# Kernel optimization log

Hardware: AMD Instinct MI355X
Metric: run time of the kernel (lower is better)

Reference implementation:

```python
import jax, jax.numpy as jnp
import numpy as np

E, H, L, B = 2048, 32, 1024, 4
S = E // H  # 64
DM, DD = 32, 64


def _ln(x, w, b, eps=1e-5):
    m = x.mean(-1, keepdims=True)
    v = ((x - m) ** 2).mean(-1, keepdims=True)
    return (x - m) / jnp.sqrt(v + eps) * w + b


def setup_inputs() -> dict:
    key = jax.random.key(0)
    ks = jax.random.split(key, 24)
    sc = 0.02  # weight scale for stability
    d = {
        'x': jax.random.normal(ks[0], (B, L, E), jnp.float32),
        'state': jax.random.normal(ks[1], (B, 2 + S, E), jnp.float32) * 0.1,
        'ln1_w': jnp.ones((E,), jnp.float32), 'ln1_b': jnp.zeros((E,), jnp.float32),
        'ln2_w': jnp.ones((E,), jnp.float32), 'ln2_b': jnp.zeros((E,), jnp.float32),
        'maa_x': jax.random.normal(ks[2], (E,), jnp.float32) * 0.1,
        'maa_w1': jax.random.normal(ks[3], (E, 5 * DM), jnp.float32) * sc,
        'maa_w2': jax.random.normal(ks[4], (5, DM, E), jnp.float32) * sc,
        'maa_stack': jax.random.normal(ks[5], (1, 5, E), jnp.float32) * 0.1,
        'time_decay': jax.random.normal(ks[6], (E,), jnp.float32) * 0.5,
        'td_w1': jax.random.normal(ks[7], (E, DD), jnp.float32) * sc,
        'td_w2': jax.random.normal(ks[8], (DD, E), jnp.float32) * sc,
        'u': jax.random.normal(ks[9], (H, S, 1), jnp.float32) * 0.1,
        'Wr': jax.random.normal(ks[10], (E, E), jnp.float32) * sc,
        'Wk': jax.random.normal(ks[11], (E, E), jnp.float32) * sc,
        'Wv': jax.random.normal(ks[12], (E, E), jnp.float32) * sc,
        'Wg': jax.random.normal(ks[13], (E, E), jnp.float32) * sc,
        'Wo': jax.random.normal(ks[14], (E, E), jnp.float32) * sc,
        'gn_w': jnp.ones((E,), jnp.float32), 'gn_b': jnp.zeros((E,), jnp.float32),
        'ffn_maa_k': jax.random.normal(ks[15], (E,), jnp.float32) * 0.1,
        'ffn_maa_r': jax.random.normal(ks[16], (E,), jnp.float32) * 0.1,
        'Wfk': jax.random.normal(ks[17], (E, E), jnp.float32) * sc,
        'Wfr': jax.random.normal(ks[18], (E, E), jnp.float32) * sc,
        'Wfv': jax.random.normal(ks[19], (E, E), jnp.float32) * sc,
    }
    return d


def _block(x, state, ln1_w, ln1_b, ln2_w, ln2_b, maa_x, maa_w1, maa_w2, maa_stack,
           time_decay, td_w1, td_w2, u, Wr, Wk, Wv, Wg, Wo, gn_w, gn_b,
           ffn_maa_k, ffn_maa_r, Wfk, Wfr, Wfv):
    b, l, e = x.shape
    h = u.shape[0]
    s_ = e // h
    # ---- time mixing (parallel over L, sequential WKV scan) ----
    xa = _ln(x, ln1_w, ln1_b)
    # token shift: sx[t] = x[t-1] - x[t], seeded from state row 1
    sx = jnp.concatenate([state[:, 1:2] - xa[:, :1], xa[:, :-1] - xa[:, 1:]], axis=1)
    xxx = jnp.tanh((xa + sx * maa_x) @ maa_w1).reshape(b, l, 5, DM)
    xxx = jnp.einsum('blfd,fde->blfe', xxx, maa_w2)            # [B,L,5,E]
    xm = xa[:, :, None] + sx[:, :, None] * (maa_stack + xxx)   # [B,L,5,E]
    xk, xw, xv, xr, xg = (xm[:, :, j] for j in range(5))       # stack order: k,w,v,r,g
    w = jnp.exp(-jnp.exp(time_decay + jnp.tanh(xw @ td_w1) @ td_w2)).reshape(b, l, h, s_)
    r = (xr @ Wr.T).reshape(b, l, h, s_)
    k = (xk @ Wk.T).reshape(b, l, h, s_)
    v = (xv @ Wv.T).reshape(b, l, h, s_)
    g = jax.nn.silu(xg @ Wg.T)                                 # [B,L,E]
    s0 = state[:, 2:2 + s_].reshape(b, h, s_, s_)              # per-head WKV state

    def step(s, rkvw):
        r_t, k_t, v_t, w_t = rkvw                              # each [B,H,S]
        a = k_t[..., :, None] * v_t[..., None, :]              # outer product [B,H,S,S]
        out = jnp.einsum('bhi,bhij->bhj', r_t, u * a + s)      # [B,H,S]
        s = a + w_t[..., :, None] * s
        return s, out

    rkvw = tuple(jnp.moveaxis(t, 1, 0) for t in (r, k, v, w))  # [L,B,H,S]
    _, out = jax.lax.scan(step, s0, rkvw)
    out = jnp.moveaxis(out, 0, 1).reshape(b, l, e)             # [B,L,E]
    # group norm over heads (eps=1e-5)
    og = out.reshape(b, l, h, s_)
    m = og.mean(-1, keepdims=True)
    va = ((og - m) ** 2).mean(-1, keepdims=True)
    og = ((og - m) / jnp.sqrt(va + 1e-5)).reshape(b, l, e) * gn_w + gn_b
    x1 = x + (og * g) @ Wo.T
    # ---- channel mixing ----
    xc = _ln(x1, ln2_w, ln2_b)
    sx2 = jnp.concatenate([state[:, 0:1] - xc[:, :1], xc[:, :-1] - xc[:, 1:]], axis=1)
    xk2 = xc + sx2 * ffn_maa_k
    xr2 = xc + sx2 * ffn_maa_r
    rr = jax.nn.sigmoid(xr2 @ Wfr.T)
    kk = jnp.square(jax.nn.relu(xk2 @ Wfk.T))
    return x1 + rr * (kk @ Wfv.T)


def reference(x, state, ln1_w, ln1_b, ln2_w, ln2_b, maa_x, maa_w1, maa_w2, maa_stack,
              time_decay, td_w1, td_w2, u, Wr, Wk, Wv, Wg, Wo, gn_w, gn_b,
              ffn_maa_k, ffn_maa_r, Wfk, Wfr, Wfv):
    return _block(x, state, ln1_w, ln1_b, ln2_w, ln2_b, maa_x, maa_w1, maa_w2, maa_stack,
                  time_decay, td_w1, td_w2, u, Wr, Wk, Wv, Wg, Wo, gn_w, gn_b,
                  ffn_maa_k, ffn_maa_r, Wfk, Wfr, Wfv)
```

## Files before the change

### kernel.cpp

```cpp
#include <hip/hip_runtime.h>


#define E     2048
#define LL    1024
#define HHH   32
#define SSS   64
#define NBL   4096
#define NBLE  8388608

typedef short bf16x8 __attribute__((ext_vector_type(8)));
typedef float f32x4  __attribute__((ext_vector_type(4)));
using u16 = unsigned short;

__device__ __forceinline__ u16 f2b(float f) {
    union { float f; unsigned int u; } c; c.f = f;
    unsigned int u = c.u;
    unsigned int r = (u + 0x7fffu + ((u >> 16) & 1u)) >> 16;
    return (u16)r;
}
__device__ __forceinline__ float b2f(u16 b) {
    union { unsigned int u; float f; } c; c.u = ((unsigned int)b) << 16; return c.f;
}

__device__ __forceinline__ float wave_sum(float v) {
#pragma unroll
    for (int m = 32; m >= 1; m >>= 1) v += __shfl_xor(v, m, 64);
    return v;
}

__device__ __forceinline__ void gl_lds16(const void* g, void* l) {
    __builtin_amdgcn_global_load_lds((const __attribute__((address_space(1))) unsigned int*)g,
                                     (__attribute__((address_space(3))) unsigned int*)l, 16, 0, 0);
}


__global__ __launch_bounds__(256) void k_convert(const float* __restrict__ in,
                                                 u16* __restrict__ out, int n) {
    int i = (blockIdx.x * 256 + threadIdx.x) * 4;
    if (i >= n) return;
    float4 v = *reinterpret_cast<const float4*>(in + i);
    ushort4 o = make_ushort4(f2b(v.x), f2b(v.y), f2b(v.z), f2b(v.w));
    *reinterpret_cast<ushort4*>(out + i) = o;
}

__global__ __launch_bounds__(256) void k_transpose(const float* __restrict__ in,
                                                   u16* __restrict__ out, int R, int C) {
    int i = blockIdx.x * 256 + threadIdx.x;
    if (i >= R * C) return;
    int r = i / C, c = i - r * C;
    out[c * R + r] = f2b(in[i]);
}

__global__ __launch_bounds__(256) void k_ln(const float* __restrict__ x,
                                            const float* __restrict__ w,
                                            const float* __restrict__ b,
                                            float* __restrict__ out) {
    int row = blockIdx.x, tid = threadIdx.x;
    const float* xr = x + (size_t)row * E + tid * 8;
    float4 v0 = *reinterpret_cast<const float4*>(xr);
    float4 v1 = *reinterpret_cast<const float4*>(xr + 4);
    float s = v0.x + v0.y + v0.z + v0.w + v1.x + v1.y + v1.z + v1.w;
    __shared__ float red[4];
    s = wave_sum(s);
    int wid = tid >> 6, lane = tid & 63;
    if (lane == 0) red[wid] = s;
    __syncthreads();
    float mean = (red[0] + red[1] + red[2] + red[3]) * (1.0f / E);
    __syncthreads();
    float q = 0.f;
    q += (v0.x - mean) * (v0.x - mean); q += (v0.y - mean) * (v0.y - mean);
    q += (v0.z - mean) * (v0.z - mean); q += (v0.w - mean) * (v0.w - mean);
    q += (v1.x - mean) * (v1.x - mean); q += (v1.y - mean) * (v1.y - mean);
    q += (v1.z - mean) * (v1.z - mean); q += (v1.w - mean) * (v1.w - mean);
    q = wave_sum(q);
    if (lane == 0) red[wid] = q;
    __syncthreads();
    float inv = rsqrtf((red[0] + red[1] + red[2] + red[3]) * (1.0f / E) + 1e-5f);
    int e = tid * 8;
    float4 w0 = *reinterpret_cast<const float4*>(w + e);
    float4 w1 = *reinterpret_cast<const float4*>(w + e + 4);
    float4 b0 = *reinterpret_cast<const float4*>(b + e);
    float4 b1 = *reinterpret_cast<const float4*>(b + e + 4);
    float4 o0, o1;
    o0.x = (v0.x - mean) * inv * w0.x + b0.x; o0.y = (v0.y - mean) * inv * w0.y + b0.y;
    o0.z = (v0.z - mean) * inv * w0.z + b0.z; o0.w = (v0.w - mean) * inv * w0.w + b0.w;
    o1.x = (v1.x - mean) * inv * w1.x + b1.x; o1.y = (v1.y - mean) * inv * w1.y + b1.y;
    o1.z = (v1.z - mean) * inv * w1.z + b1.z; o1.w = (v1.w - mean) * inv * w1.w + b1.w;
    float* op = out + (size_t)row * E + e;
    *reinterpret_cast<float4*>(op) = o0;
    *reinterpret_cast<float4*>(op + 4) = o1;
}

__global__ __launch_bounds__(256) void k_mk(const float* __restrict__ xa,
                                            const float* __restrict__ state,
                                            const float* __restrict__ maa_x,
                                            u16* __restrict__ out) {
    int i = (blockIdx.x * 256 + threadIdx.x) * 4;
    if (i >= NBLE) return;
    int n = i >> 11, e = i & (E - 1);
    int l = n & (LL - 1), b = n >> 10;
    float4 cur = *reinterpret_cast<const float4*>(xa + i);
    float4 prev;
    if (l > 0) prev = *reinterpret_cast<const float4*>(xa + i - E);
    else       prev = *reinterpret_cast<const float4*>(state + (size_t)b * 66 * E + E + e);
    float4 m = *reinterpret_cast<const float4*>(maa_x + e);
    ushort4 o = make_ushort4(f2b(cur.x + (prev.x - cur.x) * m.x),
                             f2b(cur.y + (prev.y - cur.y) * m.y),
                             f2b(cur.z + (prev.z - cur.z) * m.z),
                             f2b(cur.w + (prev.w - cur.w) * m.w));
    *reinterpret_cast<ushort4*>(out + i) = o;
}

__global__ __launch_bounds__(256) void k_mix2(const float* __restrict__ xc,
                                              const float* __restrict__ state,
                                              const float* __restrict__ mk,
                                              const float* __restrict__ mr,
                                              u16* __restrict__ xk2,
                                              u16* __restrict__ xr2) {
    int i = (blockIdx.x * 256 + threadIdx.x) * 4;
    if (i >= NBLE) return;
    int n = i >> 11, e = i & (E - 1);
    int l = n & (LL - 1), b = n >> 10;
    float4 cur = *reinterpret_cast<const float4*>(xc + i);
    float4 prev;
    if (l > 0) prev = *reinterpret_cast<const float4*>(xc + i - E);
    else       prev = *reinterpret_cast<const float4*>(state + (size_t)b * 66 * E + e);
    float4 sx = make_float4(prev.x - cur.x, prev.y - cur.y, prev.z - cur.z, prev.w - cur.w);
    float4 k4 = *reinterpret_cast<const float4*>(mk + e);
    float4 r4 = *reinterpret_cast<const float4*>(mr + e);
    ushort4 ok = make_ushort4(f2b(cur.x + sx.x * k4.x), f2b(cur.y + sx.y * k4.y),
                              f2b(cur.z + sx.z * k4.z), f2b(cur.w + sx.w * k4.w));
    ushort4 orr = make_ushort4(f2b(cur.x + sx.x * r4.x), f2b(cur.y + sx.y * r4.y),
                               f2b(cur.z + sx.z * r4.z), f2b(cur.w + sx.w * r4.w));
    *reinterpret_cast<ushort4*>(xk2 + i) = ok;
    *reinterpret_cast<ushort4*>(xr2 + i) = orr;
}

__global__ __launch_bounds__(256) void k_gnorm(const float* __restrict__ wkv,
                                               const u16* __restrict__ g,
                                               const float* __restrict__ gw,
                                               const float* __restrict__ gb,
                                               u16* __restrict__ ogg) {
    int gidx = blockIdx.x * 4 + (threadIdx.x >> 6);
    int lane = threadIdx.x & 63;
    int n = gidx >> 5, h = gidx & 31;
    size_t base = (size_t)n * E + h * SSS;
    float v = wkv[base + lane];
    float mean = wave_sum(v) * (1.0f / SSS);
    float d = v - mean;
    float var = wave_sum(d * d) * (1.0f / SSS);
    float norm = d * rsqrtf(var + 1e-5f);
    int e = h * SSS + lane;
    float res = norm * gw[e] + gb[e];
    float gv = b2f(g[base + lane]);
    ogg[base + lane] = f2b(res * gv);
}

#define CT 16

__global__ __launch_bounds__(256) void k_scan(const u16* __restrict__ Rb,
                                              const u16* __restrict__ Kb,
                                              const u16* __restrict__ Vb,
                                              const float* __restrict__ W,
                                              const float* __restrict__ state,
                                              const float* __restrict__ u,
                                              float* __restrict__ out) {
    __shared__ u16   ldsR[2][CT * 64];
    __shared__ u16   ldsK[2][CT * 64];
    __shared__ float ldsW[2][CT * 64];
    __shared__ u16   ldsV[2][CT * 16];
    const int blk = blockIdx.x;
    const int bh = blk & 127;
    const int jq = blk >> 7;
    const int b = bh >> 5, h = bh & 31;
    const int tid = threadIdx.x;
    const int wvid = tid >> 6;
    const int lane = tid & 63;
    const int ig = lane >> 2;
    const int jl = lane & 3;
    const int jv = wvid * 4 + jl;
    const int j  = jq * 16 + jv;
    const int i0 = ig * 4;
    float s[4], uu[4];
    const float* s0 = state + (size_t)b * 66 * E + 2 * E + h * (SSS * SSS);
#pragma unroll
    for (int ii = 0; ii < 4; ii++) {
        s[ii] = s0[(i0 + ii) * SSS + j];
        uu[ii] = u[h * SSS + i0 + ii];
    }
    const size_t off0 = (size_t)b * LL * E + h * SSS;

    auto stage = [&](int c, int bufsel) {
        size_t base = off0 + (size_t)c * CT * E;
        if (wvid == 0) {
            const u16* g0 = Rb + base + (size_t)(lane >> 3) * E + ((lane & 7) << 3);
            gl_lds16(g0,         &ldsR[bufsel][lane * 8]);
            gl_lds16(g0 + 8 * E, &ldsR[bufsel][512 + lane * 8]);
            if (lane < 32) {
                const u16* gv = Vb + base + (size_t)(lane >> 1) * E + jq * 16 + ((lane & 1) << 3);
                gl_lds16(gv, &ldsV[bufsel][lane * 8]);
            }
        } else if (wvid == 1) {
            const u16* g0 = Kb + base + (size_t)(lane >> 3) * E + ((lane & 7) << 3);
            gl_lds16(g0,         &ldsK[bufsel][lane * 8]);
            gl_lds16(g0 + 8 * E, &ldsK[bufsel][512 + lane * 8]);
        } else if (wvid == 2) {
            const float* g0 = W + base + (size_t)(lane >> 4) * E + ((lane & 15) << 2);
            gl_lds16(g0,         &ldsW[bufsel][lane * 4]);
            gl_lds16(g0 + 4 * E, &ldsW[bufsel][256 + lane * 4]);
        } else {
            const float* g0 = W + base + (size_t)(8 + (lane >> 4)) * E + ((lane & 15) << 2);
            gl_lds16(g0,         &ldsW[bufsel][512 + lane * 4]);
            gl_lds16(g0 + 4 * E, &ldsW[bufsel][768 + lane * 4]);
        }
    };

    stage(0, 0);
    __syncthreads();
    int cur = 0;
    for (int c = 0; c < LL / CT; c++) {
        if (c + 1 < LL / CT) stage(c + 1, cur ^ 1);
        float accs[CT];
#pragma unroll
        for (int tt = 0; tt < CT; tt++) {
            ushort4 rv = *reinterpret_cast<const ushort4*>(&ldsR[cur][tt * 64 + i0]);
            ushort4 kv = *reinterpret_cast<const ushort4*>(&ldsK[cur][tt * 64 + i0]);
            float4  wv = *reinterpret_cast<const float4*>(&ldsW[cur][tt * 64 + i0]);
            float vj = b2f(ldsV[cur][tt * 16 + jv]);
            float acc = 0.f, a;
            a = b2f(kv.x) * vj; acc += b2f(rv.x) * fmaf(uu[0], a, s[0]); s[0] = fmaf(wv.x, s[0], a);
            a = b2f(kv.y) * vj; acc += b2f(rv.y) * fmaf(uu[1], a, s[1]); s[1] = fmaf(wv.y, s[1], a);
            a = b2f(kv.z) * vj; acc += b2f(rv.z) * fmaf(uu[2], a, s[2]); s[2] = fmaf(wv.z, s[2], a);
            a = b2f(kv.w) * vj; acc += b2f(rv.w) * fmaf(uu[3], a, s[3]); s[3] = fmaf(wv.w, s[3], a);
            accs[tt] = acc;
        }
#pragma unroll
        for (int tt = 0; tt < CT; tt++) accs[tt] += __shfl_xor(accs[tt], 4, 64);
#pragma unroll
        for (int tt = 0; tt < CT; tt++) accs[tt] += __shfl_xor(accs[tt], 8, 64);
#pragma unroll
        for (int tt = 0; tt < CT; tt++) accs[tt] += __shfl_xor(accs[tt], 16, 64);
#pragma unroll
        for (int tt = 0; tt < CT; tt++) accs[tt] += __shfl_xor(accs[tt], 32, 64);
        if (ig == 0) {
            size_t offt = off0 + (size_t)c * CT * E + j;
#pragma unroll
            for (int tt = 0; tt < CT; tt++) out[offt + (size_t)tt * E] = accs[tt];
        }
        __syncthreads();
        cur ^= 1;
    }
}

template <int EP>
__global__ __launch_bounds__(256) void k_gemm128(const u16* __restrict__ A, int lda,
                                                 const u16* __restrict__ Bw,
                                                 void* __restrict__ C, int K,
                                                 const float* __restrict__ evec,
                                                 const float* __restrict__ emat1,
                                                 const float* __restrict__ emat2) {
    __shared__ u16 As[128 * 32];
    __shared__ u16 Bs[128 * 32];
    const int tid = threadIdx.x;
    const int m0 = blockIdx.y << 7, n0 = blockIdx.x << 7;
    const int srow = tid >> 2;
    const int scol = (((tid & 3) ^ ((srow >> 1) & 3)) << 3);
    const int wv = tid >> 6, lane = tid & 63;
    const int wy = (wv >> 1) << 6, wx = (wv & 1) << 6;
    const int lr = lane & 15, lq = lane >> 4;
    const int cofs = ((lq ^ ((lr >> 1) & 3)) << 3);
    f32x4 acc[4][4];
#pragma unroll
    for (int a = 0; a < 4; a++)
#pragma unroll
        for (int bq = 0; bq < 4; bq++) acc[a][bq] = {0.f, 0.f, 0.f, 0.f};
    const u16* gA = A + (size_t)(m0 + srow) * lda + scol;
    const u16* gB = Bw + (size_t)(n0 + srow) * K + scol;
    u16* lA = As + srow * 32 + ((tid & 3) << 3);
    u16* lB = Bs + srow * 32 + ((tid & 3) << 3);
    for (int k0 = 0; k0 < K; k0 += 32) {
        gl_lds16(gA + k0, lA);
        gl_lds16(gA + (size_t)64 * lda + k0, lA + 64 * 32);
        gl_lds16(gB + k0, lB);
        gl_lds16(gB + (size_t)64 * K + k0, lB + 64 * 32);
        __syncthreads();
        bf16x8 af[4], bfr[4];
#pragma unroll
        for (int mt = 0; mt < 4; mt++)
            af[mt] = *reinterpret_cast<const bf16x8*>(As + (wy + mt * 16 + lr) * 32 + cofs);
#pragma unroll
        for (int nt = 0; nt < 4; nt++)
            bfr[nt] = *reinterpret_cast<const bf16x8*>(Bs + (wx + nt * 16 + lr) * 32 + cofs);
#pragma unroll
        for (int mt = 0; mt < 4; mt++)
#pragma unroll
            for (int nt = 0; nt < 4; nt++)
                acc[mt][nt] = __builtin_amdgcn_mfma_f32_16x16x32_bf16(af[mt], bfr[nt], acc[mt][nt], 0, 0, 0);
        __syncthreads();
    }
    const int gmb = m0 + wy + (lq << 2);
    const int gnb = n0 + wx + lr;
#pragma unroll
    for (int mt = 0; mt < 4; mt++) {
#pragma unroll
        for (int nt = 0; nt < 4; nt++) {
            int gn = gnb + nt * 16;
#pragma unroll
            for (int i = 0; i < 4; i++) {
                int gm = gmb + mt * 16 + i;
                size_t idx = (size_t)gm * E + gn;
                float v = acc[mt][nt][i];
                if constexpr (EP == 2) {
                    int l = gm & (LL - 1), bb = gm >> 10;
                    float cur = emat1[idx];
                    float prev = (l > 0) ? emat1[idx - E]
                                         : emat2[(size_t)bb * 66 * E + E + gn];
                    ((u16*)C)[idx] = f2b(cur + (prev - cur) * (evec[gn] + v));
                }
                else if constexpr (EP == 3) ((float*)C)[idx] = expf(-expf(evec[gn] + v));
                else if constexpr (EP == 5) ((float*)C)[idx] = emat1[idx] + v;
                else if constexpr (EP == 6) ((float*)C)[idx] = 1.f / (1.f + expf(-v));
                else if constexpr (EP == 7) { float t = fmaxf(v, 0.f); ((u16*)C)[idx] = f2b(t * t); }
                else if constexpr (EP == 8) ((float*)C)[idx] = emat1[idx] + emat2[idx] * v;
                else if constexpr (EP == 9) ((u16*)C)[idx] = f2b(v);
                else if constexpr (EP == 10) { float sg = 1.f / (1.f + expf(-v)); ((u16*)C)[idx] = f2b(v * sg); }
            }
        }
    }
}

#define BK  32
#define LDP 40

template <int EP>
__global__ __launch_bounds__(256) void k_gemm(const u16* __restrict__ A, int lda,
                                              const u16* __restrict__ Bw,
                                              void* __restrict__ C,
                                              int M, int N, int K) {
    __shared__ u16 As[64 * LDP];
    __shared__ u16 Bs[64 * LDP];
    const int tid = threadIdx.x;
    const int m0 = blockIdx.y << 6, n0 = blockIdx.x << 6;
    const int srow = tid >> 2, skc = (tid & 3) << 3;
    const int lane = tid & 63, wv = tid >> 6;
    const int wr = (wv >> 1) << 5, wc = (wv & 1) << 5;
    const int lr = lane & 15, lq = lane >> 4;
    f32x4 acc[2][2];
#pragma unroll
    for (int a = 0; a < 2; a++)
#pragma unroll
        for (int bq = 0; bq < 2; bq++) acc[a][bq] = {0.f, 0.f, 0.f, 0.f};
    const u16* aptr = A + (size_t)(m0 + srow) * lda + skc;
    const u16* bptr = Bw + (size_t)(n0 + srow) * K + skc;
    const bool bvalid = (n0 + srow) < N;
    for (int k0 = 0; k0 < K; k0 += BK) {
        float4 av = *reinterpret_cast<const float4*>(aptr + k0);
        float4 bv = bvalid ? *reinterpret_cast<const float4*>(bptr + k0)
                           : make_float4(0.f, 0.f, 0.f, 0.f);
        __syncthreads();
        *reinterpret_cast<float4*>(As + srow * LDP + skc) = av;
        *reinterpret_cast<float4*>(Bs + srow * LDP + skc) = bv;
        __syncthreads();
        bf16x8 a0 = *reinterpret_cast<const bf16x8*>(As + (wr + lr) * LDP + lq * 8);
        bf16x8 a1 = *reinterpret_cast<const bf16x8*>(As + (wr + 16 + lr) * LDP + lq * 8);
        bf16x8 b0 = *reinterpret_cast<const bf16x8*>(Bs + (wc + lr) * LDP + lq * 8);
        bf16x8 b1 = *reinterpret_cast<const bf16x8*>(Bs + (wc + 16 + lr) * LDP + lq * 8);
        acc[0][0] = __builtin_amdgcn_mfma_f32_16x16x32_bf16(a0, b0, acc[0][0], 0, 0, 0);
        acc[0][1] = __builtin_amdgcn_mfma_f32_16x16x32_bf16(a0, b1, acc[0][1], 0, 0, 0);
        acc[1][0] = __builtin_amdgcn_mfma_f32_16x16x32_bf16(a1, b0, acc[1][0], 0, 0, 0);
        acc[1][1] = __builtin_amdgcn_mfma_f32_16x16x32_bf16(a1, b1, acc[1][1], 0, 0, 0);
    }
    const int gmb = m0 + wr + lq * 4;
    const int gnb = n0 + wc + lr;
#pragma unroll
    for (int mi = 0; mi < 2; mi++) {
#pragma unroll
        for (int ni = 0; ni < 2; ni++) {
            int gn = gnb + ni * 16;
            if (gn >= N) continue;
#pragma unroll
            for (int i = 0; i < 4; i++) {
                int gm = gmb + mi * 16 + i;
                size_t idx = (size_t)gm * N + gn;
                float v = acc[mi][ni][i];
                if constexpr (EP == 1) ((u16*)C)[idx] = f2b(tanhf(v));
            }
        }
    }
}


extern "C" void kernel_launch(void* const* d_in, const int* in_sizes, int n_in,
                              void* d_out, int out_size, void* d_ws, size_t ws_size,
                              hipStream_t stream) {
    const float* x          = (const float*)d_in[0];
    const float* state      = (const float*)d_in[1];
    const float* ln1_w      = (const float*)d_in[2];
    const float* ln1_b      = (const float*)d_in[3];
    const float* ln2_w      = (const float*)d_in[4];
    const float* ln2_b      = (const float*)d_in[5];
    const float* maa_x      = (const float*)d_in[6];
    const float* maa_w1     = (const float*)d_in[7];
    const float* maa_w2     = (const float*)d_in[8];
    const float* maa_stack  = (const float*)d_in[9];
    const float* time_decay = (const float*)d_in[10];
    const float* td_w1      = (const float*)d_in[11];
    const float* td_w2      = (const float*)d_in[12];
    const float* u          = (const float*)d_in[13];
    const float* Wr         = (const float*)d_in[14];
    const float* Wk         = (const float*)d_in[15];
    const float* Wv         = (const float*)d_in[16];
    const float* Wg         = (const float*)d_in[17];
    const float* Wo         = (const float*)d_in[18];
    const float* gn_w       = (const float*)d_in[19];
    const float* gn_b       = (const float*)d_in[20];
    const float* ffn_k      = (const float*)d_in[21];
    const float* ffn_r      = (const float*)d_in[22];
    const float* Wfk        = (const float*)d_in[23];
    const float* Wfr        = (const float*)d_in[24];
    const float* Wfv        = (const float*)d_in[25];

    char* ws = (char*)d_ws;
    float* R0 = (float*)(ws);
    float* R1 = (float*)(ws + 33554432);
    u16*   R2 = (u16*)(ws + 67108864);
    u16*   R3 = (u16*)(ws + 83886080);
    u16*   R4 = (u16*)(ws + 100663296);
    u16*   R5 = (u16*)(ws + 117440512);
    u16*   R6 = (u16*)(ws + 134217728);
    u16*   WB = (u16*)(ws + 150994944);
    u16*   Hx = (u16*)(ws + 159383552);
    u16*   Ht = (u16*)(ws + 160694272);
    u16*  WT1 = (u16*)(ws + 161218560);
    u16*  WT2 = (u16*)(ws + 161873920);
    u16*  WT3 = (u16*)(ws + 162529280);
    u16*  WT4 = (u16*)(ws + 162791424);

    dim3 blk(256);
    dim3 g128(16, 32);
    dim3 g160(3, 64), g64(1, 64);
    const int ncv = (E * E / 4) / 256;
    const int nel = NBLE / 1024;

    k_transpose<<<(E * 160 + 255) / 256, blk, 0, stream>>>(maa_w1, WT1, E, 160);
    for (int f = 0; f < 5; f++)
        k_transpose<<<(32 * E + 255) / 256, blk, 0, stream>>>(maa_w2 + f * 32 * E, WT2 + f * E * 32, 32, E);
    k_transpose<<<(E * 64 + 255) / 256, blk, 0, stream>>>(td_w1, WT3, E, 64);
    k_transpose<<<(64 * E + 255) / 256, blk, 0, stream>>>(td_w2, WT4, 64, E);

    k_ln<<<NBL, blk, 0, stream>>>(x, ln1_w, ln1_b, R0);
    k_mk<<<nel, blk, 0, stream>>>(R0, state, maa_x, R2);
    k_gemm<1><<<g160, blk, 0, stream>>>(R2, E, WT1, Hx, NBL, 160, E);

    k_gemm128<2><<<g128, blk, 0, stream>>>(Hx + 1 * 32, 160, WT2 + 1 * E * 32, R2, 32,
                                           maa_stack + 1 * E, R0, state);
    k_gemm<1><<<g64, blk, 0, stream>>>(R2, E, WT3, Ht, NBL, 64, E);
    k_gemm128<3><<<g128, blk, 0, stream>>>(Ht, 64, WT4, R1, 64, time_decay, nullptr, nullptr);

    k_gemm128<2><<<g128, blk, 0, stream>>>(Hx + 0 * 32, 160, WT2 + 0 * E * 32, R2, 32,
                                           maa_stack + 0 * E, R0, state);
    k_convert<<<ncv, blk, 0, stream>>>(Wk, WB, E * E);
    k_gemm128<9><<<g128, blk, 0, stream>>>(R2, E, WB, R4, E, nullptr, nullptr, nullptr);

    k_gemm128<2><<<g128, blk, 0, stream>>>(Hx + 2 * 32, 160, WT2 + 2 * E * 32, R2, 32,
                                           maa_stack + 2 * E, R0, state);
    k_convert<<<ncv, blk, 0, stream>>>(Wv, WB, E * E);
    k_gemm128<9><<<g128, blk, 0, stream>>>(R2, E, WB, R5, E, nullptr, nullptr, nullptr);

    k_gemm128<2><<<g128, blk, 0, stream>>>(Hx + 4 * 32, 160, WT2 + 4 * E * 32, R2, 32,
                                           maa_stack + 4 * E, R0, state);
    k_convert<<<ncv, blk, 0, stream>>>(Wg, WB, E * E);
    k_gemm128<10><<<g128, blk, 0, stream>>>(R2, E, WB, R6, E, nullptr, nullptr, nullptr);

    k_gemm128<2><<<g128, blk, 0, stream>>>(Hx + 3 * 32, 160, WT2 + 3 * E * 32, R2, 32,
                                           maa_stack + 3 * E, R0, state);
    k_convert<<<ncv, blk, 0, stream>>>(Wr, WB, E * E);
    k_gemm128<9><<<g128, blk, 0, stream>>>(R2, E, WB, R3, E, nullptr, nullptr, nullptr);

    k_scan<<<512, blk, 0, stream>>>(R3, R4, R5, R1, state, u, R0);
    k_gnorm<<<NBL * HHH / 4, blk, 0, stream>>>(R0, R6, gn_w, gn_b, R6);

    k_convert<<<ncv, blk, 0, stream>>>(Wo, WB, E * E);
    k_gemm128<5><<<g128, blk, 0, stream>>>(R6, E, WB, R0, E, nullptr, x, nullptr);

    k_ln<<<NBL, blk, 0, stream>>>(R0, ln2_w, ln2_b, R1);
    k_mix2<<<nel, blk, 0, stream>>>(R1, state, ffn_k, ffn_r, R2, R3);
    k_convert<<<ncv, blk, 0, stream>>>(Wfk, WB, E * E);
    k_gemm128<7><<<g128, blk, 0, stream>>>(R2, E, WB, R4, E, nullptr, nullptr, nullptr);
    k_convert<<<ncv, blk, 0, stream>>>(Wfr, WB, E * E);
    k_gemm128<6><<<g128, blk, 0, stream>>>(R3, E, WB, R1, E, nullptr, nullptr, nullptr);
    k_convert<<<ncv, blk, 0, stream>>>(Wfv, WB, E * E);
    k_gemm128<8><<<g128, blk, 0, stream>>>(R4, E, WB, (float*)d_out, E, nullptr, R0, R1);
}
```

Before: 1.102 ms.

## Add 256x128-tile double-buffered GEMM kernel for all 2048x2048 projections

Adds a new GEMM kernel with 512 threads and a 256x128 output tile. It uses a 64-wide K step, double-buffered LDS filled through direct global-to-LDS loads, an XOR swizzle, and a block-index remap for L2 locality. All eight E x E projection GEMMs (r, k, v, g, o, and the three FFN ones) now use it, and their epilogues move out of the 128-tile kernel. The larger tile raises arithmetic intensity and overlaps the next tile's loads with MFMA work. In exchange it launches only 256 blocks and uses more LDS and registers per block, which may limit occupancy and wave balance across CUs.

```diff
diff --git a/kernel.cpp b/kernel.cpp
--- a/kernel.cpp
+++ b/kernel.cpp
@@ -253,6 +253,114 @@
 }
 
 template <int EP>
+__global__ __launch_bounds__(512, 2) void k_gemm256(const u16* __restrict__ A,
+                                                    const u16* __restrict__ Bw,
+                                                    void* __restrict__ C,
+                                                    const float* __restrict__ emat1,
+                                                    const float* __restrict__ emat2) {
+    __shared__ u16 As[2][256 * 64];
+    __shared__ u16 Bs[2][128 * 64];
+    const int tid = threadIdx.x;
+    const int bid = blockIdx.x;
+    const int sw = (bid & 7) * 32 + (bid >> 3);
+    const int m0 = (sw >> 4) << 8;
+    const int n0 = (sw & 15) << 7;
+    const int srow = tid >> 3;
+    const int schunk = (tid & 7) ^ (srow & 7);
+    const u16* gA = A + (size_t)(m0 + srow) * E + schunk * 8;
+    const u16* gB = Bw + (size_t)(n0 + srow) * E + schunk * 8;
+    u16* lA = &As[0][0] + tid * 8;
+    u16* lB = &Bs[0][0] + tid * 8;
+
+    const int wv = tid >> 6, lane = tid & 63;
+    const int wm = wv >> 2, wn = wv & 3;
+    const int lr = lane & 15, lq = lane >> 4;
+    const int c0 = ((lq ^ (lr & 7)) << 3);
+    const int c1 = (((4 + lq) ^ (lr & 7)) << 3);
+    const int arow = wm * 128 + lr;
+    const int brow = wn * 32 + lr;
+
+    f32x4 acc[8][2];
+#pragma unroll
+    for (int mt = 0; mt < 8; mt++)
+#pragma unroll
+        for (int nt = 0; nt < 2; nt++) acc[mt][nt] = {0.f, 0.f, 0.f, 0.f};
+
+    auto stage = [&](int kt, int buf) {
+        const u16* a = gA + kt * 64;
+        const u16* b = gB + kt * 64;
+        u16* la = lA + buf * (256 * 64);
+        u16* lb = lB + buf * (128 * 64);
+        gl_lds16(a,                 la);
+        gl_lds16(a + (size_t)64  * E, la + 64 * 64);
+        gl_lds16(a + (size_t)128 * E, la + 128 * 64);
+        gl_lds16(a + (size_t)192 * E, la + 192 * 64);
+        gl_lds16(b,                 lb);
+        gl_lds16(b + (size_t)64  * E, lb + 64 * 64);
+    };
+
+    stage(0, 0);
+    int cur = 0;
+    for (int kt = 0; kt < E / 64; kt++) {
+        if (kt + 1 < E / 64) {
+            stage(kt + 1, cur ^ 1);
+            asm volatile("s_waitcnt vmcnt(6)" ::: "memory");
+        } else {
+            asm volatile("s_waitcnt vmcnt(0)" ::: "memory");
+        }
+        __builtin_amdgcn_s_barrier();
+        const u16* as = &As[0][0] + cur * (256 * 64);
+        const u16* bs = &Bs[0][0] + cur * (128 * 64);
+        bf16x8 af0[8], af1[8], bf0[2], bf1[2];
+#pragma unroll
+        for (int mt = 0; mt < 8; mt++) {
+            af0[mt] = *reinterpret_cast<const bf16x8*>(as + (arow + mt * 16) * 64 + c0);
+            af1[mt] = *reinterpret_cast<const bf16x8*>(as + (arow + mt * 16) * 64 + c1);
+        }
+#pragma unroll
+        for (int nt = 0; nt < 2; nt++) {
+            bf0[nt] = *reinterpret_cast<const bf16x8*>(bs + (brow + nt * 16) * 64 + c0);
+            bf1[nt] = *reinterpret_cast<const bf16x8*>(bs + (brow + nt * 16) * 64 + c1);
+        }
+        asm volatile("s_waitcnt lgkmcnt(0)" ::: "memory");
+        __builtin_amdgcn_s_barrier();
+        __builtin_amdgcn_s_setprio(1);
+#pragma unroll
+        for (int mt = 0; mt < 8; mt++) {
+#pragma unroll
+            for (int nt = 0; nt < 2; nt++) {
+                acc[mt][nt] = __builtin_amdgcn_mfma_f32_16x16x32_bf16(af0[mt], bf0[nt], acc[mt][nt], 0, 0, 0);
+                acc[mt][nt] = __builtin_amdgcn_mfma_f32_16x16x32_bf16(af1[mt], bf1[nt], acc[mt][nt], 0, 0, 0);
+            }
+        }
+        __builtin_amdgcn_s_setprio(0);
+        cur ^= 1;
+    }
+
+    const int gmb = m0 + wm * 128 + (lq << 2);
+    const int gnb = n0 + wn * 32 + lr;
+#pragma unroll
+    for (int mt = 0; mt < 8; mt++) {
+#pragma unroll
+        for (int nt = 0; nt < 2; nt++) {
+            int gn = gnb + nt * 16;
+#pragma unroll
+            for (int i = 0; i < 4; i++) {
+                int gm = gmb + mt * 16 + i;
+                size_t idx = (size_t)gm * E + gn;
+                float v = acc[mt][nt][i];
+                if constexpr (EP == 5) ((float*)C)[idx] = emat1[idx] + v;
+                else if constexpr (EP == 6) ((float*)C)[idx] = 1.f / (1.f + expf(-v));
+                else if constexpr (EP == 7) { float t = fmaxf(v, 0.f); ((u16*)C)[idx] = f2b(t * t); }
+                else if constexpr (EP == 8) ((float*)C)[idx] = emat1[idx] + emat2[idx] * v;
+                else if constexpr (EP == 9) ((u16*)C)[idx] = f2b(v);
+                else if constexpr (EP == 10) { float sg = 1.f / (1.f + expf(-v)); ((u16*)C)[idx] = f2b(v * sg); }
+            }
+        }
+    }
+}
+
+template <int EP>
 __global__ __launch_bounds__(256) void k_gemm128(const u16* __restrict__ A, int lda,
                                                  const u16* __restrict__ Bw,
                                                  void* __restrict__ C, int K,
@@ -318,12 +426,6 @@
                     ((u16*)C)[idx] = f2b(cur + (prev - cur) * (evec[gn] + v));
                 }
                 else if constexpr (EP == 3) ((float*)C)[idx] = expf(-expf(evec[gn] + v));
-                else if constexpr (EP == 5) ((float*)C)[idx] = emat1[idx] + v;
-                else if constexpr (EP == 6) ((float*)C)[idx] = 1.f / (1.f + expf(-v));
-                else if constexpr (EP == 7) { float t = fmaxf(v, 0.f); ((u16*)C)[idx] = f2b(t * t); }
-                else if constexpr (EP == 8) ((float*)C)[idx] = emat1[idx] + emat2[idx] * v;
-                else if constexpr (EP == 9) ((u16*)C)[idx] = f2b(v);
-                else if constexpr (EP == 10) { float sg = 1.f / (1.f + expf(-v)); ((u16*)C)[idx] = f2b(v * sg); }
             }
         }
     }
@@ -437,6 +539,8 @@
     u16*  WT4 = (u16*)(ws + 162791424);
 
     dim3 blk(256);
+    dim3 blk512(512);
+    dim3 g256(256);
     dim3 g128(16, 32);
     dim3 g160(3, 64), g64(1, 64);
     const int ncv = (E * E / 4) / 256;
@@ -460,35 +564,35 @@
     k_gemm128<2><<<g128, blk, 0, stream>>>(Hx + 0 * 32, 160, WT2 + 0 * E * 32, R2, 32,
                                            maa_stack + 0 * E, R0, state);
     k_convert<<<ncv, blk, 0, stream>>>(Wk, WB, E * E);
-    k_gemm128<9><<<g128, blk, 0, stream>>>(R2, E, WB, R4, E, nullptr, nullptr, nullptr);
+    k_gemm256<9><<<g256, blk512, 0, stream>>>(R2, WB, R4, nullptr, nullptr);
 
     k_gemm128<2><<<g128, blk, 0, stream>>>(Hx + 2 * 32, 160, WT2 + 2 * E * 32, R2, 32,
                                            maa_stack + 2 * E, R0, state);
     k_convert<<<ncv, blk, 0, stream>>>(Wv, WB, E * E);
-    k_gemm128<9><<<g128, blk, 0, stream>>>(R2, E, WB, R5, E, nullptr, nullptr, nullptr);
+    k_gemm256<9><<<g256, blk512, 0, stream>>>(R2, WB, R5, nullptr, nullptr);
 
     k_gemm128<2><<<g128, blk, 0, stream>>>(Hx + 4 * 32, 160, WT2 + 4 * E * 32, R2, 32,
                                            maa_stack + 4 * E, R0, state);
     k_convert<<<ncv, blk, 0, stream>>>(Wg, WB, E * E);
-    k_gemm128<10><<<g128, blk, 0, stream>>>(R2, E, WB, R6, E, nullptr, nullptr, nullptr);
+    k_gemm256<10><<<g256, blk512, 0, stream>>>(R2, WB, R6, nullptr, nullptr);
 
     k_gemm128<2><<<g128, blk, 0, stream>>>(Hx + 3 * 32, 160, WT2 + 3 * E * 32, R2, 32,
                                            maa_stack + 3 * E, R0, state);
     k_convert<<<ncv, blk, 0, stream>>>(Wr, WB, E * E);
-    k_gemm128<9><<<g128, blk, 0, stream>>>(R2, E, WB, R3, E, nullptr, nullptr, nullptr);
+    k_gemm256<9><<<g256, blk512, 0, stream>>>(R2, WB, R3, nullptr, nullptr);
 
     k_scan<<<512, blk, 0, stream>>>(R3, R4, R5, R1, state, u, R0);
     k_gnorm<<<NBL * HHH / 4, blk, 0, stream>>>(R0, R6, gn_w, gn_b, R6);
 
     k_convert<<<ncv, blk, 0, stream>>>(Wo, WB, E * E);
-    k_gemm128<5><<<g128, blk, 0, stream>>>(R6, E, WB, R0, E, nullptr, x, nullptr);
+    k_gemm256<5><<<g256, blk512, 0, stream>>>(R6, WB, R0, x, nullptr);
 
     k_ln<<<NBL, blk, 0, stream>>>(R0, ln2_w, ln2_b, R1);
     k_mix2<<<nel, blk, 0, stream>>>(R1, state, ffn_k, ffn_r, R2, R3);
     k_convert<<<ncv, blk, 0, stream>>>(Wfk, WB, E * E);
-    k_gemm128<7><<<g128, blk, 0, stream>>>(R2, E, WB, R4, E, nullptr, nullptr, nullptr);
+    k_gemm256<7><<<g256, blk512, 0, stream>>>(R2, WB, R4, nullptr, nullptr);
     k_convert<<<ncv, blk, 0, stream>>>(Wfr, WB, E * E);
-    k_gemm128<6><<<g128, blk, 0, stream>>>(R3, E, WB, R1, E, nullptr, nullptr, nullptr);
+    k_gemm256<6><<<g256, blk512, 0, stream>>>(R3, WB, R1, nullptr, nullptr);
     k_convert<<<ncv, blk, 0, stream>>>(Wfv, WB, E * E);
-    k_gemm128<8><<<g128, blk, 0, stream>>>(R4, E, WB, (float*)d_out, E, nullptr, R0, R1);
-}
+    k_gemm256<8><<<g256, blk512, 0, stream>>>(R4, WB, (float*)d_out, R0, R1);
+}
```

Measured after the change: 1.145 ms. 3.9% more time.
